# Performance work log

Measured on AMD Instinct MI355X. Metric: run time of the kernel, lower is better.

The kernel has to match this reference:

```python
import jax, jax.numpy as jnp
import numpy as np

B, S, D, H, F = 16, 512, 1024, 16, 4096
DH = D // H
LN_EPS = 1e-12


def layer_norm(x, g, b):
    mu = jnp.mean(x, axis=-1, keepdims=True)
    var = jnp.mean(jnp.square(x - mu), axis=-1, keepdims=True)
    return (x - mu) * jax.lax.rsqrt(var + LN_EPS) * g + b


def setup_inputs() -> dict:
    key = jax.random.key(0)
    ks = jax.random.split(key, 16)
    s_attn = 1.0 / np.sqrt(D)
    s_ffn = 1.0 / np.sqrt(F)
    return {
        "hidden_states": jax.random.normal(ks[0], (B, S, D), jnp.float32),
        "attention_mask": jnp.zeros((B, S), jnp.float32),
        # weights stored [in, out]
        "Wq": jax.random.normal(ks[1], (D, D), jnp.float32) * s_attn,
        "bq": jnp.zeros((D,), jnp.float32),
        "Wk": jax.random.normal(ks[2], (D, D), jnp.float32) * s_attn,
        "bk": jnp.zeros((D,), jnp.float32),
        "Wv": jax.random.normal(ks[3], (D, D), jnp.float32) * s_attn,
        "bv": jnp.zeros((D,), jnp.float32),
        "Wo": jax.random.normal(ks[4], (D, D), jnp.float32) * s_attn,
        "bo": jnp.zeros((D,), jnp.float32),
        "ln1_g": jnp.ones((D,), jnp.float32),
        "ln1_b": jnp.zeros((D,), jnp.float32),
        "Wi": jax.random.normal(ks[5], (D, F), jnp.float32) * s_attn,
        "bi": jnp.zeros((F,), jnp.float32),
        "Wo2": jax.random.normal(ks[6], (F, D), jnp.float32) * s_ffn,
        "bo2": jnp.zeros((D,), jnp.float32),
        "ln2_g": jnp.ones((D,), jnp.float32),
        "ln2_b": jnp.zeros((D,), jnp.float32),
    }


def reference(hidden_states, attention_mask, Wq, bq, Wk, bk, Wv, bv, Wo, bo,
              ln1_g, ln1_b, Wi, bi, Wo2, bo2, ln2_g, ln2_b):
    x = hidden_states
    # --- self attention ---
    q = (x @ Wq + bq).reshape(B, S, H, DH)
    k = (x @ Wk + bk).reshape(B, S, H, DH)
    v = (x @ Wv + bv).reshape(B, S, H, DH)
    scores = jnp.einsum("bqhd,bkhd->bhqk", q, k) / np.sqrt(DH)
    scores = scores + attention_mask[:, None, None, :]
    probs = jax.nn.softmax(scores, axis=-1)  # dropout p=0 (eval)
    ctx = jnp.einsum("bhqk,bkhd->bqhd", probs, v).reshape(B, S, D)
    # --- self output: dense + residual + LN ---
    attn_out = layer_norm(ctx @ Wo + bo + x, ln1_g, ln1_b)
    # --- intermediate: dense + gelu (exact erf gelu, BERT) ---
    inter = jax.nn.gelu(attn_out @ Wi + bi, approximate=False)
    # --- output: dense + residual + LN ---
    out = layer_norm(inter @ Wo2 + bo2 + attn_out, ln2_g, ln2_b)
    return out
```

## Files before the change

### kernel.cpp

```cpp
#include <hip/hip_runtime.h>
#include <hip/hip_bf16.h>
#include <math.h>

#define DEV_INLINE __device__ __forceinline__

typedef __attribute__((ext_vector_type(8))) short bf16x8;
typedef __attribute__((ext_vector_type(8))) unsigned short u16x8;
typedef __attribute__((ext_vector_type(4))) float f32x4;


DEV_INLINE void gload_lds16(const void* g, void* l) {
  __builtin_amdgcn_global_load_lds(
      (__attribute__((address_space(1))) unsigned int*)const_cast<void*>(g),
      (__attribute__((address_space(3))) unsigned int*)l,
      16, 0, 0);
}

DEV_INLINE unsigned lds_a(const void* p) {
  return (unsigned)(unsigned long long)(__attribute__((address_space(3))) const void*)p;
}

DEV_INLINE short f2bs(float x) {
  union { __hip_bfloat16 h; short s; } u;
  u.h = __float2bfloat16(x);
  return u.s;
}

DEV_INLINE f32x4 mfma16(bf16x8 a, bf16x8 b, f32x4 c) {
  return __builtin_amdgcn_mfma_f32_16x16x32_bf16(a, b, c, 0, 0, 0);
}

#define DSREAD_O(dst, base, imm) \
  asm volatile("ds_read_b128 %0, %1 offset:%2" : "=v"(dst) : "v"(base), "n"(imm))


__global__ __launch_bounds__(256)
void cvt_x_bf16(const float* __restrict__ in, __hip_bfloat16* __restrict__ out) {
  const size_t i = ((size_t)blockIdx.x * 256 + threadIdx.x) * 4;
  const float4 x = *(const float4*)(in + i);
  union { __hip_bfloat16 h[4]; ushort4 u; } pk;
  pk.h[0] = __float2bfloat16(x.x);
  pk.h[1] = __float2bfloat16(x.y);
  pk.h[2] = __float2bfloat16(x.z);
  pk.h[3] = __float2bfloat16(x.w);
  *(ushort4*)(out + i) = pk.u;
}

__global__ __launch_bounds__(256)
void transpose_w(const float* __restrict__ W, __hip_bfloat16* __restrict__ Wt, int K, int N) {
  __shared__ float t[32][33];
  const int n0 = blockIdx.x * 32, k0 = blockIdx.y * 32;
  const int tx = threadIdx.x & 31, ty = threadIdx.x >> 5;
#pragma unroll
  for (int r = ty; r < 32; r += 8)
    t[r][tx] = W[(size_t)(k0 + r) * N + n0 + tx];
  __syncthreads();
#pragma unroll
  for (int r = ty; r < 32; r += 8)
    Wt[(size_t)(n0 + r) * K + k0 + tx] = __float2bfloat16(t[tx][r]);
}

__global__ __launch_bounds__(256)
void concat_bias(const float* __restrict__ a, const float* __restrict__ b,
                 const float* __restrict__ c, float* __restrict__ o) {
  const int i = blockIdx.x * 256 + threadIdx.x;
  o[i] = a[i]; o[1024 + i] = b[i]; o[2048 + i] = c[i];
}


template<int MODE>
DEV_INLINE void gemm64_body(const short* __restrict__ A, const short* __restrict__ Bt,
                            const float* __restrict__ bias, const float* __restrict__ resid,
                            __hip_bfloat16* __restrict__ Cb, float* __restrict__ Cf,
                            int M, int N, int K)
{
  __shared__ __align__(128) short lds[32768];

  const int tid = threadIdx.x;
  const int lane = tid & 63, w = tid >> 6;
  const int q4 = lane >> 4, c16 = lane & 15;
  const int wm = (w >> 1) * 64, wn = (w & 1) * 64;

  const int nNT = N >> 7;
  int bid = blockIdx.x;
  { const int cpx = (int)gridDim.x >> 3; bid = (bid & 7) * cpx + (bid >> 3); }
  const int bm = (bid / nNT) * 128;
  const int bn = (bid % nNT) * 128;

  const int sr = tid >> 3, sl = tid & 7;
  const int sg = (sl ^ (sr & 7)) * 8;
  const short* pA = A  + (size_t)(bm + sr) * K + sg;
  const short* pB = Bt + (size_t)(bn + sr) * K + sg;

  const int s0 = (q4 ^ (c16 & 7)) * 16;
  const int s1 = ((q4 ^ 4) ^ (c16 & 7)) * 16;
  unsigned aRd0 = lds_a(lds) + (unsigned)((wm + c16) * 128 + s0);
  unsigned aRd1 = lds_a(lds) + (unsigned)((wm + c16) * 128 + s1);
  unsigned bRd0 = lds_a(lds) + (unsigned)(16384 + (wn + c16) * 128 + s0);
  unsigned bRd1 = lds_a(lds) + (unsigned)(16384 + (wn + c16) * 128 + s1);

  f32x4 acc[4][4];
#pragma unroll
  for (int i = 0; i < 4; ++i)
#pragma unroll
    for (int j = 0; j < 4; ++j) acc[i][j] = (f32x4){0.f, 0.f, 0.f, 0.f};

  auto stage = [&](int buf, int kt) {
    char* b = (char*)lds + buf * 32768;
#pragma unroll
    for (int u = 0; u < 4; ++u) {
      gload_lds16(pA + (size_t)u * 32 * K + kt, b + u * 4096 + w * 1024);
      gload_lds16(pB + (size_t)u * 32 * K + kt, b + 16384 + u * 4096 + w * 1024);
    }
  };

  stage(0, 0);
  __syncthreads();

  const int NT = K >> 6;
  int cur = 0;
  for (int t = 0; t < NT; ++t) {
    __builtin_amdgcn_sched_barrier(0);
    if (t + 1 < NT) stage(cur ^ 1, (t + 1) << 6);
    __builtin_amdgcn_sched_barrier(0);

    bf16x8 a0, a1, a2, a3, a4, a5, a6, a7;
    bf16x8 b0, b1, b2, b3, b4, b5, b6, b7;
    DSREAD_O(a0, aRd0, 0 * 2048); DSREAD_O(a1, aRd0, 1 * 2048);
    DSREAD_O(a2, aRd0, 2 * 2048); DSREAD_O(a3, aRd0, 3 * 2048);
    DSREAD_O(b0, bRd0, 0 * 2048); DSREAD_O(b1, bRd0, 1 * 2048);
    DSREAD_O(b2, bRd0, 2 * 2048); DSREAD_O(b3, bRd0, 3 * 2048);
    DSREAD_O(a4, aRd1, 0 * 2048); DSREAD_O(a5, aRd1, 1 * 2048);
    DSREAD_O(a6, aRd1, 2 * 2048); DSREAD_O(a7, aRd1, 3 * 2048);
    DSREAD_O(b4, bRd1, 0 * 2048); DSREAD_O(b5, bRd1, 1 * 2048);
    DSREAD_O(b6, bRd1, 2 * 2048); DSREAD_O(b7, bRd1, 3 * 2048);

    asm volatile("s_waitcnt lgkmcnt(0)");
    __builtin_amdgcn_sched_barrier(0);
    __builtin_amdgcn_s_setprio(1);
    acc[0][0] = mfma16(a0, b0, acc[0][0]); acc[0][1] = mfma16(a0, b1, acc[0][1]);
    acc[0][2] = mfma16(a0, b2, acc[0][2]); acc[0][3] = mfma16(a0, b3, acc[0][3]);
    acc[1][0] = mfma16(a1, b0, acc[1][0]); acc[1][1] = mfma16(a1, b1, acc[1][1]);
    acc[1][2] = mfma16(a1, b2, acc[1][2]); acc[1][3] = mfma16(a1, b3, acc[1][3]);
    acc[2][0] = mfma16(a2, b0, acc[2][0]); acc[2][1] = mfma16(a2, b1, acc[2][1]);
    acc[2][2] = mfma16(a2, b2, acc[2][2]); acc[2][3] = mfma16(a2, b3, acc[2][3]);
    acc[3][0] = mfma16(a3, b0, acc[3][0]); acc[3][1] = mfma16(a3, b1, acc[3][1]);
    acc[3][2] = mfma16(a3, b2, acc[3][2]); acc[3][3] = mfma16(a3, b3, acc[3][3]);
    acc[0][0] = mfma16(a4, b4, acc[0][0]); acc[0][1] = mfma16(a4, b5, acc[0][1]);
    acc[0][2] = mfma16(a4, b6, acc[0][2]); acc[0][3] = mfma16(a4, b7, acc[0][3]);
    acc[1][0] = mfma16(a5, b4, acc[1][0]); acc[1][1] = mfma16(a5, b5, acc[1][1]);
    acc[1][2] = mfma16(a5, b6, acc[1][2]); acc[1][3] = mfma16(a5, b7, acc[1][3]);
    acc[2][0] = mfma16(a6, b4, acc[2][0]); acc[2][1] = mfma16(a6, b5, acc[2][1]);
    acc[2][2] = mfma16(a6, b6, acc[2][2]); acc[2][3] = mfma16(a6, b7, acc[2][3]);
    acc[3][0] = mfma16(a7, b4, acc[3][0]); acc[3][1] = mfma16(a7, b5, acc[3][1]);
    acc[3][2] = mfma16(a7, b6, acc[3][2]); acc[3][3] = mfma16(a7, b7, acc[3][3]);
    __builtin_amdgcn_s_setprio(0);

    __syncthreads();
    aRd0 ^= 0x8000; aRd1 ^= 0x8000; bRd0 ^= 0x8000; bRd1 ^= 0x8000; cur ^= 1;
  }

  float* eb = (float*)((char*)lds + w * 4352);
  const int erow = lane >> 2, ecol = (lane & 3) * 16;
#pragma unroll
  for (int mf = 0; mf < 4; ++mf) {
#pragma unroll
    for (int nf = 0; nf < 4; ++nf) {
      const int col = bn + wn + nf * 16 + c16;
      const float bsv = bias[col];
#pragma unroll
      for (int j = 0; j < 4; ++j) {
        float v = acc[mf][nf][j] + bsv;
        if constexpr (MODE == 2)
          v = 0.5f * v * (1.0f + erff(v * 0.70710678118654752f));
        eb[(q4 * 4 + j) * 68 + nf * 16 + c16] = v;
      }
    }
    const int gr = bm + wm + mf * 16 + erow;
    const size_t gbase = (size_t)gr * N + bn + wn + ecol;
    if constexpr (MODE == 1) {
#pragma unroll
      for (int u = 0; u < 4; ++u) {
        float4 t = *(float4*)&eb[erow * 68 + ecol + u * 4];
        const float4 r = *(const float4*)&resid[gbase + u * 4];
        t.x += r.x; t.y += r.y; t.z += r.z; t.w += r.w;
        *(float4*)&Cf[gbase + u * 4] = t;
      }
    } else {
      unsigned short* cp = (unsigned short*)Cb;
#pragma unroll
      for (int u = 0; u < 2; ++u) {
        float4 a = *(float4*)&eb[erow * 68 + ecol + u * 8];
        float4 b = *(float4*)&eb[erow * 68 + ecol + u * 8 + 4];
        u16x8 o;
        o[0] = (unsigned short)f2bs(a.x); o[1] = (unsigned short)f2bs(a.y);
        o[2] = (unsigned short)f2bs(a.z); o[3] = (unsigned short)f2bs(a.w);
        o[4] = (unsigned short)f2bs(b.x); o[5] = (unsigned short)f2bs(b.y);
        o[6] = (unsigned short)f2bs(b.z); o[7] = (unsigned short)f2bs(b.w);
        *(u16x8*)(cp + gbase + u * 8) = o;
      }
    }
  }
}

__global__ __launch_bounds__(256)
void gemm_qkv(const short* A, const short* Bt, const float* bias,
              __hip_bfloat16* Cb, int M, int N, int K) {
  gemm64_body<0>(A, Bt, bias, nullptr, Cb, nullptr, M, N, K);
}
__global__ __launch_bounds__(256)
void gemm_wo(const short* A, const short* Bt, const float* bias,
             const float* resid, float* Cf, int M, int N, int K) {
  gemm64_body<1>(A, Bt, bias, resid, nullptr, Cf, M, N, K);
}
__global__ __launch_bounds__(256)
void gemm_wi(const short* A, const short* Bt, const float* bias,
             __hip_bfloat16* Cb, int M, int N, int K) {
  gemm64_body<2>(A, Bt, bias, nullptr, Cb, nullptr, M, N, K);
}
__global__ __launch_bounds__(256)
void gemm_wo2(const short* A, const short* Bt, const float* bias,
              const float* resid, float* Cf, int M, int N, int K) {
  gemm64_body<1>(A, Bt, bias, resid, nullptr, Cf, M, N, K);
}


__global__ __launch_bounds__(256)
void attn_flash(const short* __restrict__ Q, const short* __restrict__ Kmat,
                const short* __restrict__ V, const float* __restrict__ mask,
                __hip_bfloat16* __restrict__ ctx, int qs)
{
  __shared__ short Ksm[64 * 64];
  __shared__ short Vsm[64 * 64];
  __shared__ short Psm[4 * 16 * 64];

  const int tid = threadIdx.x;
  const int lane = tid & 63;
  const int w = tid >> 6;
  const int q4 = lane >> 4;
  const int c16 = lane & 15;
  const int b = blockIdx.z;
  const int h = blockIdx.y;
  const int qb = blockIdx.x;

  const size_t rowbase = (size_t)b * 512;
  const int hoff = h * 64;

  bf16x8 aq[2];
  {
    const size_t qrow = rowbase + (size_t)qb * 64 + w * 16 + c16;
    const short* qp = Q + qrow * qs + hoff + q4 * 8;
    aq[0] = *(const bf16x8*)(qp);
    aq[1] = *(const bf16x8*)(qp + 32);
  }

  float m_r[4], l_r[4];
  f32x4 O[4];
#pragma unroll
  for (int j = 0; j < 4; ++j) { m_r[j] = -INFINITY; l_r[j] = 0.f; O[j] = (f32x4){0.f, 0.f, 0.f, 0.f}; }

  const int kc0 = w * 128 + lane;
  const int kp0 = kc0 >> 3, kd0 = (kc0 & 7) * 8;
  const int kc1 = kc0 + 64;
  const int kp1 = kc1 >> 3, kd1 = (kc1 & 7) * 8;

  for (int kv0 = 0; kv0 < 512; kv0 += 64) {
    __syncthreads();
    gload_lds16(Kmat + (rowbase + kv0 + kp0) * qs + hoff + (kd0 ^ ((kp0 & 7) << 3)),
                (char*)Ksm + (size_t)(w * 128 + 0) * 16);
    gload_lds16(Kmat + (rowbase + kv0 + kp1) * qs + hoff + (kd1 ^ ((kp1 & 7) << 3)),
                (char*)Ksm + (size_t)(w * 128 + 64) * 16);
#pragma unroll
    for (int it = 0; it < 2; ++it) {
      const int c = tid + 256 * it;
      const int kp = c >> 3;
      const int dh8 = (c & 7) * 8;
      const bf16x8 vv = *(const bf16x8*)(V + (rowbase + kv0 + kp) * qs + hoff + dh8);
#pragma unroll
      for (int j = 0; j < 8; ++j) {
        const int dh = dh8 + j;
        *(short*)((char*)Vsm + dh * 128 + ((kp * 2) ^ ((dh & 7) << 4))) = vv[j];
      }
    }
    __syncthreads();

    float pv[4][4];
    float mk[4];
#pragma unroll
    for (int t = 0; t < 4; ++t) mk[t] = mask[rowbase + kv0 + t * 16 + c16];
#pragma unroll
    for (int t = 0; t < 4; ++t) {
      f32x4 z = (f32x4){0.f, 0.f, 0.f, 0.f};
      const int kp = t * 16 + c16;
#pragma unroll
      for (int ks = 0; ks < 2; ++ks) {
        const int d = ks * 32 + q4 * 8;
        bf16x8 kf = *(const bf16x8*)((char*)Ksm + kp * 128 + ((d * 2) ^ ((kp & 7) << 4)));
        z = mfma16(aq[ks], kf, z);
      }
#pragma unroll
      for (int j = 0; j < 4; ++j) pv[t][j] = z[j] * 0.125f + mk[t];
    }

#pragma unroll
    for (int j = 0; j < 4; ++j) {
      float mt_ = fmaxf(fmaxf(pv[0][j], pv[1][j]), fmaxf(pv[2][j], pv[3][j]));
#pragma unroll
      for (int o = 8; o >= 1; o >>= 1) mt_ = fmaxf(mt_, __shfl_xor(mt_, o));
      const float mn = fmaxf(m_r[j], mt_);
      const float sc = __expf(m_r[j] - mn);
      float rs = 0.f;
#pragma unroll
      for (int t = 0; t < 4; ++t) { const float pe = __expf(pv[t][j] - mn); pv[t][j] = pe; rs += pe; }
#pragma unroll
      for (int o = 8; o >= 1; o >>= 1) rs += __shfl_xor(rs, o);
      l_r[j] = l_r[j] * sc + rs;
      m_r[j] = mn;
#pragma unroll
      for (int nt = 0; nt < 4; ++nt) O[nt][j] *= sc;
    }

    char* pb = (char*)Psm + w * 2048;
#pragma unroll
    for (int j = 0; j < 4; ++j) {
      const int r = q4 * 4 + j;
#pragma unroll
      for (int t = 0; t < 4; ++t) {
        const int ck = t * 16 + c16;
        *(short*)(pb + r * 128 + ((ck * 2) ^ ((r & 7) << 4))) = f2bs(pv[t][j]);
      }
    }

#pragma unroll
    for (int ks = 0; ks < 2; ++ks) {
      const int kk = ks * 32 + q4 * 8;
      bf16x8 pa = *(const bf16x8*)(pb + c16 * 128 + ((kk * 2) ^ ((c16 & 7) << 4)));
#pragma unroll
      for (int nt = 0; nt < 4; ++nt) {
        const int dh = nt * 16 + c16;
        bf16x8 vf = *(const bf16x8*)((char*)Vsm + dh * 128 + ((kk * 2) ^ ((dh & 7) << 4)));
        O[nt] = mfma16(pa, vf, O[nt]);
      }
    }
  }

  float rinv[4];
#pragma unroll
  for (int j = 0; j < 4; ++j) rinv[j] = 1.0f / l_r[j];
#pragma unroll
  for (int nt = 0; nt < 4; ++nt) {
#pragma unroll
    for (int j = 0; j < 4; ++j) {
      const size_t row = rowbase + (size_t)qb * 64 + w * 16 + q4 * 4 + j;
      ctx[row * 1024 + hoff + nt * 16 + c16] = __float2bfloat16(O[nt][j] * rinv[j]);
    }
  }
}


DEV_INLINE void ln_body(const float* __restrict__ in, const float* __restrict__ gam,
                        const float* __restrict__ bet, float* __restrict__ outf,
                        __hip_bfloat16* __restrict__ outb)
{
  const int row = blockIdx.x;
  const int tid = threadIdx.x;
  const size_t base = (size_t)row * 1024 + tid * 4;
  const float4 x = *(const float4*)(in + base);
  float s  = x.x + x.y + x.z + x.w;
  float s2 = x.x * x.x + x.y * x.y + x.z * x.z + x.w * x.w;
#pragma unroll
  for (int o = 32; o >= 1; o >>= 1) { s += __shfl_xor(s, o); s2 += __shfl_xor(s2, o); }
  __shared__ float sb[8];
  const int w = tid >> 6;
  if ((tid & 63) == 0) { sb[w] = s; sb[w + 4] = s2; }
  __syncthreads();
  const float ts  = sb[0] + sb[1] + sb[2] + sb[3];
  const float ts2 = sb[4] + sb[5] + sb[6] + sb[7];
  const float mu = ts * (1.0f / 1024.0f);
  const float var = ts2 * (1.0f / 1024.0f) - mu * mu;
  const float rstd = rsqrtf(var + 1e-12f);
  const float4 g4 = *(const float4*)(gam + tid * 4);
  const float4 b4 = *(const float4*)(bet + tid * 4);
  const float y0 = (x.x - mu) * rstd * g4.x + b4.x;
  const float y1 = (x.y - mu) * rstd * g4.y + b4.y;
  const float y2 = (x.z - mu) * rstd * g4.z + b4.z;
  const float y3 = (x.w - mu) * rstd * g4.w + b4.w;
  if (outf) {
    float4 y; y.x = y0; y.y = y1; y.z = y2; y.w = y3;
    *(float4*)(outf + base) = y;
  }
  if (outb) {
    union { __hip_bfloat16 h[4]; ushort4 u; } pk;
    pk.h[0] = __float2bfloat16(y0);
    pk.h[1] = __float2bfloat16(y1);
    pk.h[2] = __float2bfloat16(y2);
    pk.h[3] = __float2bfloat16(y3);
    *(ushort4*)(outb + base) = pk.u;
  }
}

__global__ __launch_bounds__(256)
void ln_attn(const float* in, const float* gam, const float* bet,
             float* outf, __hip_bfloat16* outb) { ln_body(in, gam, bet, outf, outb); }
__global__ __launch_bounds__(256)
void ln_ffn(const float* in, const float* gam, const float* bet, float* outf) {
  ln_body(in, gam, bet, outf, nullptr);
}


extern "C" void kernel_launch(void* const* d_in, const int* in_sizes, int n_in,
                              void* d_out, int out_size, void* d_ws, size_t ws_size,
                              hipStream_t stream)
{
  const float* X    = (const float*)d_in[0];
  const float* mask = (const float*)d_in[1];
  const float* Wq   = (const float*)d_in[2];   const float* bq  = (const float*)d_in[3];
  const float* Wk   = (const float*)d_in[4];   const float* bk  = (const float*)d_in[5];
  const float* Wv   = (const float*)d_in[6];   const float* bv  = (const float*)d_in[7];
  const float* Wo   = (const float*)d_in[8];   const float* bo  = (const float*)d_in[9];
  const float* g1   = (const float*)d_in[10];  const float* b1  = (const float*)d_in[11];
  const float* Wi   = (const float*)d_in[12];  const float* bi  = (const float*)d_in[13];
  const float* Wo2  = (const float*)d_in[14];  const float* bo2 = (const float*)d_in[15];
  const float* g2   = (const float*)d_in[16];  const float* b2  = (const float*)d_in[17];
  float* out = (float*)d_out;
  (void)in_sizes; (void)n_in; (void)out_size; (void)ws_size;

  const size_t D = 1024, F = 4096;
  const size_t MN = 8192 * D;

  char* p = (char*)d_ws;
  auto alloc = [&](size_t bytes) { char* r = p; p += (bytes + 255) & ~(size_t)255; return r; };
  short* Xb    = (short*)alloc(MN * 2);
  short* QKVb  = (short*)alloc(8192 * 3072 * 2);
  short* WqkvT = (short*)alloc(3072 * D * 2);
  short* WoT   = (short*)alloc(D * D * 2);
  short* WiT   = (short*)alloc(D * F * 2);
  short* Wo2T  = (short*)alloc(D * F * 2);
  float* bqkv  = (float*)alloc(3072 * 4);
  float* A1f   = (float*)alloc(MN * 4);
  short* I1    = (short*)alloc(8192 * F * 2);

  cvt_x_bf16<<<dim3((unsigned)(MN / 1024)), 256, 0, stream>>>(X, (__hip_bfloat16*)Xb);
  transpose_w<<<dim3(32, 32),  256, 0, stream>>>(Wq,  (__hip_bfloat16*)(WqkvT + 0),           1024, 1024);
  transpose_w<<<dim3(32, 32),  256, 0, stream>>>(Wk,  (__hip_bfloat16*)(WqkvT + 1024 * 1024), 1024, 1024);
  transpose_w<<<dim3(32, 32),  256, 0, stream>>>(Wv,  (__hip_bfloat16*)(WqkvT + 2048 * 1024), 1024, 1024);
  transpose_w<<<dim3(32, 32),  256, 0, stream>>>(Wo,  (__hip_bfloat16*)WoT,  1024, 1024);
  transpose_w<<<dim3(128, 32), 256, 0, stream>>>(Wi,  (__hip_bfloat16*)WiT,  1024, 4096);
  transpose_w<<<dim3(32, 128), 256, 0, stream>>>(Wo2, (__hip_bfloat16*)Wo2T, 4096, 1024);
  concat_bias<<<dim3(4), 256, 0, stream>>>(bq, bk, bv, bqkv);

  gemm_qkv<<<dim3(1536), 256, 0, stream>>>(Xb, WqkvT, bqkv, (__hip_bfloat16*)QKVb, 8192, 3072, 1024);

  attn_flash<<<dim3(8, 16, 16), 256, 0, stream>>>(QKVb, QKVb + 1024, QKVb + 2048, mask,
                                                  (__hip_bfloat16*)Xb, 3072);

  gemm_wo<<<dim3(512), 256, 0, stream>>>(Xb, WoT, bo, X, out, 8192, 1024, 1024);
  ln_attn<<<dim3(8192), 256, 0, stream>>>(out, g1, b1, A1f, (__hip_bfloat16*)QKVb);

  gemm_wi<<<dim3(2048), 256, 0, stream>>>(QKVb, WiT, bi, (__hip_bfloat16*)I1, 8192, 4096, 1024);

  gemm_wo2<<<dim3(512), 256, 0, stream>>>(I1, Wo2T, bo2, A1f, out, 8192, 1024, 4096);
  ln_ffn<<<dim3(8192), 256, 0, stream>>>(out, g2, b2, out);
}
```

Measured before the change: 422.8 us.

## Use 256x128 eight-wave GEMM tiles for QKV and FFN-up projections

Adds a new GEMM body that runs 512 threads (8 waves) per block and computes a 256x128 output tile with a 64-wide K step. The tile is staged through XOR-swizzled LDS using direct global-to-LDS loads. The QKV and Wi (GELU) GEMMs switch to this kernel with half as many blocks, so each loaded B tile is reused across twice as many rows and global/LDS traffic per FLOP drops. The trade-offs are a larger LDS footprint (48 KB) and a single-buffered loop with two barriers per K step and no prefetch, which can lower occupancy and leave load latency exposed.

```diff
diff --git a/kernel.cpp b/kernel.cpp
--- a/kernel.cpp
+++ b/kernel.cpp
@@ -65,6 +65,103 @@
                  const float* __restrict__ c, float* __restrict__ o) {
   const int i = blockIdx.x * 256 + threadIdx.x;
   o[i] = a[i]; o[1024 + i] = b[i]; o[2048 + i] = c[i];
+}
+
+
+template<int MODE>
+DEV_INLINE void gemm256_body(const short* __restrict__ A, const short* __restrict__ Bt,
+                             const float* __restrict__ bias,
+                             __hip_bfloat16* __restrict__ Cb,
+                             int M, int N, int K)
+{
+  __shared__ __align__(128) short lds[24576];
+
+  const int tid = threadIdx.x;
+  const int lane = tid & 63, wid = tid >> 6;
+  const int q4 = lane >> 4, c16 = lane & 15;
+  const int wm = (wid >> 1) * 64, wn = (wid & 1) * 64;
+
+  const int nNT = N >> 7;
+  int bid = blockIdx.x;
+  { const int cpx = (int)gridDim.x >> 3; bid = (bid & 7) * cpx + (bid >> 3); }
+  const int bm = (bid / nNT) * 256;
+  const int bn = (bid % nNT) * 128;
+
+  const int sr = tid >> 3, sl = tid & 7;
+  const int sg = (sl ^ (sr & 7)) * 8;
+  const short* pA = A  + (size_t)(bm + sr) * K + sg;
+  const short* pB = Bt + (size_t)(bn + sr) * K + sg;
+  char* const baseA = (char*)lds;
+  char* const baseB = (char*)lds + 32768;
+
+  f32x4 acc[4][4];
+#pragma unroll
+  for (int i = 0; i < 4; ++i)
+#pragma unroll
+    for (int j = 0; j < 4; ++j) acc[i][j] = (f32x4){0.f, 0.f, 0.f, 0.f};
+
+  for (int kt = 0; kt < K; kt += 64) {
+    __syncthreads();
+#pragma unroll
+    for (int u = 0; u < 4; ++u)
+      gload_lds16(pA + (size_t)u * 64 * K + kt, baseA + u * 8192 + wid * 1024);
+#pragma unroll
+    for (int u = 0; u < 2; ++u)
+      gload_lds16(pB + (size_t)u * 64 * K + kt, baseB + u * 8192 + wid * 1024);
+    __syncthreads();
+
+#pragma unroll
+    for (int kk = 0; kk < 2; ++kk) {
+      bf16x8 af[4], bfr[4];
+#pragma unroll
+      for (int mt = 0; mt < 4; ++mt)
+        af[mt] = *(const bf16x8*)(baseA + (wm + mt * 16 + c16) * 128 +
+                                  (((kk * 4 + q4) ^ (c16 & 7)) * 16));
+#pragma unroll
+      for (int nt = 0; nt < 4; ++nt)
+        bfr[nt] = *(const bf16x8*)(baseB + (wn + nt * 16 + c16) * 128 +
+                                   (((kk * 4 + q4) ^ (c16 & 7)) * 16));
+#pragma unroll
+      for (int mt = 0; mt < 4; ++mt)
+#pragma unroll
+        for (int nt = 0; nt < 4; ++nt)
+          acc[mt][nt] = mfma16(af[mt], bfr[nt], acc[mt][nt]);
+    }
+  }
+
+  __syncthreads();
+
+  float* eb = (float*)((char*)lds + wid * 4352);
+  const int erow = lane >> 2, ecol = (lane & 3) * 16;
+#pragma unroll
+  for (int mf = 0; mf < 4; ++mf) {
+#pragma unroll
+    for (int nf = 0; nf < 4; ++nf) {
+      const int col = bn + wn + nf * 16 + c16;
+      const float bsv = bias[col];
+#pragma unroll
+      for (int j = 0; j < 4; ++j) {
+        float v = acc[mf][nf][j] + bsv;
+        if constexpr (MODE == 2)
+          v = 0.5f * v * (1.0f + erff(v * 0.70710678118654752f));
+        eb[(q4 * 4 + j) * 68 + nf * 16 + c16] = v;
+      }
+    }
+    const int gr = bm + wm + mf * 16 + erow;
+    const size_t gbase = (size_t)gr * N + bn + wn + ecol;
+    unsigned short* cp = (unsigned short*)Cb;
+#pragma unroll
+    for (int u = 0; u < 2; ++u) {
+      float4 a = *(float4*)&eb[erow * 68 + ecol + u * 8];
+      float4 b = *(float4*)&eb[erow * 68 + ecol + u * 8 + 4];
+      u16x8 o;
+      o[0] = (unsigned short)f2bs(a.x); o[1] = (unsigned short)f2bs(a.y);
+      o[2] = (unsigned short)f2bs(a.z); o[3] = (unsigned short)f2bs(a.w);
+      o[4] = (unsigned short)f2bs(b.x); o[5] = (unsigned short)f2bs(b.y);
+      o[6] = (unsigned short)f2bs(b.z); o[7] = (unsigned short)f2bs(b.w);
+      *(u16x8*)(cp + gbase + u * 8) = o;
+    }
+  }
 }
 
 
@@ -203,20 +300,20 @@
   }
 }
 
-__global__ __launch_bounds__(256)
+__global__ __launch_bounds__(512)
 void gemm_qkv(const short* A, const short* Bt, const float* bias,
               __hip_bfloat16* Cb, int M, int N, int K) {
-  gemm64_body<0>(A, Bt, bias, nullptr, Cb, nullptr, M, N, K);
+  gemm256_body<0>(A, Bt, bias, Cb, M, N, K);
+}
+__global__ __launch_bounds__(512)
+void gemm_wi(const short* A, const short* Bt, const float* bias,
+             __hip_bfloat16* Cb, int M, int N, int K) {
+  gemm256_body<2>(A, Bt, bias, Cb, M, N, K);
 }
 __global__ __launch_bounds__(256)
 void gemm_wo(const short* A, const short* Bt, const float* bias,
              const float* resid, float* Cf, int M, int N, int K) {
   gemm64_body<1>(A, Bt, bias, resid, nullptr, Cf, M, N, K);
-}
-__global__ __launch_bounds__(256)
-void gemm_wi(const short* A, const short* Bt, const float* bias,
-             __hip_bfloat16* Cb, int M, int N, int K) {
-  gemm64_body<2>(A, Bt, bias, nullptr, Cb, nullptr, M, N, K);
 }
 __global__ __launch_bounds__(256)
 void gemm_wo2(const short* A, const short* Bt, const float* bias,
@@ -449,7 +546,7 @@
   transpose_w<<<dim3(32, 128), 256, 0, stream>>>(Wo2, (__hip_bfloat16*)Wo2T, 4096, 1024);
   concat_bias<<<dim3(4), 256, 0, stream>>>(bq, bk, bv, bqkv);
 
-  gemm_qkv<<<dim3(1536), 256, 0, stream>>>(Xb, WqkvT, bqkv, (__hip_bfloat16*)QKVb, 8192, 3072, 1024);
+  gemm_qkv<<<dim3(768), 512, 0, stream>>>(Xb, WqkvT, bqkv, (__hip_bfloat16*)QKVb, 8192, 3072, 1024);
 
   attn_flash<<<dim3(8, 16, 16), 256, 0, stream>>>(QKVb, QKVb + 1024, QKVb + 2048, mask,
                                                   (__hip_bfloat16*)Xb, 3072);
@@ -457,7 +554,7 @@
   gemm_wo<<<dim3(512), 256, 0, stream>>>(Xb, WoT, bo, X, out, 8192, 1024, 1024);
   ln_attn<<<dim3(8192), 256, 0, stream>>>(out, g1, b1, A1f, (__hip_bfloat16*)QKVb);
 
-  gemm_wi<<<dim3(2048), 256, 0, stream>>>(QKVb, WiT, bi, (__hip_bfloat16*)I1, 8192, 4096, 1024);
+  gemm_wi<<<dim3(1024), 512, 0, stream>>>(QKVb, WiT, bi, (__hip_bfloat16*)I1, 8192, 4096, 1024);
 
   gemm_wo2<<<dim3(512), 256, 0, stream>>>(I1, Wo2T, bo2, A1f, out, 8192, 1024, 4096);
   ln_ffn<<<dim3(8192), 256, 0, stream>>>(out, g2, b2, out);
```

Measured after the change: 395.3 us. 1.07x faster.
